# Optimization experiments

Hardware: AMD Instinct MI355X
Metric: run time of the kernel (lower is better)

## Reference

```python
import jax, jax.numpy as jnp
import numpy as np

D_MODEL = 1024
N_HEADS = 16
D_K = D_MODEL // N_HEADS  # 64


def setup_inputs() -> dict:
    key = jax.random.key(0)
    ks = jax.random.split(key, 12)
    B, S = 2, 2048
    inp = {
        "query": jax.random.normal(ks[0], (B, S, D_MODEL), jnp.float32),
        "key": jax.random.normal(ks[1], (B, S, D_MODEL), jnp.float32),
        "value": jax.random.normal(ks[2], (B, S, D_MODEL), jnp.float32),
        "mask": jnp.ones((B, 1, S, S), jnp.int32),
    }
    sc = 1.0 / np.sqrt(D_MODEL)
    inp["Wq"] = jax.random.normal(ks[3], (D_MODEL, D_MODEL), jnp.float32) * sc
    inp["bq"] = jnp.zeros((D_MODEL,), jnp.float32)
    inp["Wk"] = jax.random.normal(ks[4], (D_MODEL, D_MODEL), jnp.float32) * sc
    inp["bk"] = jnp.zeros((D_MODEL,), jnp.float32)
    inp["Wv"] = jax.random.normal(ks[5], (D_MODEL, D_MODEL), jnp.float32) * sc
    inp["bv"] = jnp.zeros((D_MODEL,), jnp.float32)
    inp["Wo"] = jax.random.normal(ks[6], (D_MODEL, D_MODEL), jnp.float32) * sc
    inp["bo"] = jnp.zeros((D_MODEL,), jnp.float32)
    return inp


def reference(query, key, value, mask, Wq, bq, Wk, bk, Wv, bv, Wo, bo):
    B, Sq, _ = query.shape
    H, dk = N_HEADS, D_K
    # linear projections, split heads: (B,S,D) -> (B,H,S,dk)
    def split_heads(x):
        return x.reshape(B, -1, H, dk).transpose(0, 2, 1, 3)
    Q = split_heads(query @ Wq.T + bq)
    K = split_heads(key @ Wk.T + bk)
    V = split_heads(value @ Wv.T + bv)
    scale = 1.0 / jnp.sqrt(jnp.asarray(dk, jnp.float32))
    scores = jnp.einsum('bhqd,bhkd->bhqk', Q, K) * scale
    scores = jnp.where(mask == 0, jnp.asarray(-1e9, scores.dtype), scores)
    attn = jax.nn.softmax(scores, axis=-1)  # (B,H,Sq,Sk)
    out = jnp.einsum('bhqk,bhkd->bhqd', attn, V)
    out = out.transpose(0, 2, 1, 3).reshape(B, Sq, D_MODEL)
    out = out @ Wo.T + bo
    return out, attn
```

## Files before the change

### kernel.cpp

```cpp
#include <hip/hip_runtime.h>
#include <cstdint>
#include <cstddef>

#define DEV __device__ __forceinline__

typedef float f32x4 __attribute__((ext_vector_type(4)));
typedef __bf16 bf16x8 __attribute__((ext_vector_type(8)));
typedef unsigned short u16x8 __attribute__((ext_vector_type(8)));

static constexpr int D = 1024, H = 16, DK = 64, S = 2048, B = 2;
static constexpr int M_TOT = B * S;
static constexpr size_t OUT0 = (size_t)M_TOT * D;

DEV unsigned short f2bf(float f) {
  unsigned x = __builtin_bit_cast(unsigned, f);
  unsigned r = (x + 0x7fffu + ((x >> 16) & 1u)) >> 16;
  return (unsigned short)r;
}

DEV float bf2f(unsigned short u) {
  return __builtin_bit_cast(float, (unsigned)u << 16);
}

DEV f32x4 mfma_bf16(bf16x8 a, bf16x8 b, f32x4 c) {
  return __builtin_amdgcn_mfma_f32_16x16x32_bf16(a, b, c, 0, 0, 0);
}

DEV bf16x8 bc(u16x8 u) { return __builtin_bit_cast(bf16x8, u); }

template <int MODE, bool ABF16>
DEV void proj_body(unsigned short* As, unsigned short* Bs, const void* Aptr,
                   const unsigned short* W, const float* bias, void* dst) {
  constexpr int BM = 128, BK = 32, LDT = 40;
  const int tid = threadIdx.x;
  const int lane = tid & 63, wave = tid >> 6;
  const int wrow = wave >> 1, wcol = wave & 1;
  const int l15 = lane & 15, kg = lane >> 4;
  const int m0 = blockIdx.y * BM, n0 = blockIdx.x * BM;
  const int srow = tid >> 1, scb = (tid & 1) * 16;

  f32x4 acc[4][4] = {};

  for (int kt = 0; kt < D; kt += BK) {
    {
      u16x8 t0, t1;
      if constexpr (ABF16) {
        const unsigned short* ap =
            (const unsigned short*)Aptr + (size_t)(m0 + srow) * D + kt + scb;
        t0 = *(const u16x8*)ap;
        t1 = *(const u16x8*)(ap + 8);
      } else {
        const float* ap = (const float*)Aptr + (size_t)(m0 + srow) * D + kt + scb;
        float4 v0 = *(const float4*)(ap + 0);
        float4 v1 = *(const float4*)(ap + 4);
        float4 v2 = *(const float4*)(ap + 8);
        float4 v3 = *(const float4*)(ap + 12);
        t0[0] = f2bf(v0.x); t0[1] = f2bf(v0.y); t0[2] = f2bf(v0.z); t0[3] = f2bf(v0.w);
        t0[4] = f2bf(v1.x); t0[5] = f2bf(v1.y); t0[6] = f2bf(v1.z); t0[7] = f2bf(v1.w);
        t1[0] = f2bf(v2.x); t1[1] = f2bf(v2.y); t1[2] = f2bf(v2.z); t1[3] = f2bf(v2.w);
        t1[4] = f2bf(v3.x); t1[5] = f2bf(v3.y); t1[6] = f2bf(v3.z); t1[7] = f2bf(v3.w);
      }
      *(u16x8*)&As[srow * LDT + scb] = t0;
      *(u16x8*)&As[srow * LDT + scb + 8] = t1;

      const unsigned short* wp = W + (size_t)(n0 + srow) * D + kt + scb;
      *(u16x8*)&Bs[srow * LDT + scb] = *(const u16x8*)wp;
      *(u16x8*)&Bs[srow * LDT + scb + 8] = *(const u16x8*)(wp + 8);
    }
    __syncthreads();

    bf16x8 a[4], b[4];
#pragma unroll
    for (int i = 0; i < 4; i++)
      a[i] = bc(*(const u16x8*)&As[(wrow * 64 + i * 16 + l15) * LDT + kg * 8]);
#pragma unroll
    for (int i = 0; i < 4; i++)
      b[i] = bc(*(const u16x8*)&Bs[(wcol * 64 + i * 16 + l15) * LDT + kg * 8]);
#pragma unroll
    for (int mi = 0; mi < 4; mi++)
#pragma unroll
      for (int ni = 0; ni < 4; ni++) acc[mi][ni] = mfma_bf16(a[mi], b[ni], acc[mi][ni]);
    __syncthreads();
  }

#pragma unroll
  for (int mi = 0; mi < 4; mi++) {
#pragma unroll
    for (int ni = 0; ni < 4; ni++) {
      const int n = n0 + wcol * 64 + ni * 16 + l15;
      const float bval = bias[n];
#pragma unroll
      for (int r = 0; r < 4; r++) {
        const int m = m0 + wrow * 64 + mi * 16 + kg * 4 + r;
        float v = acc[mi][ni][r] + bval;
        if constexpr (MODE == 0) v *= 0.125f;
        if constexpr (MODE == 0 || MODE == 1) {
          const int b_ = m >> 11, s = m & (S - 1), h = n >> 6, d_ = n & (DK - 1);
          ((unsigned short*)dst)[(((size_t)(b_ * H + h)) * S + s) * DK + d_] = f2bf(v);
        } else if constexpr (MODE == 2) {
          const int b_ = m >> 11, s = m & (S - 1), h = n >> 6, d_ = n & (DK - 1);
          ((unsigned short*)dst)[(((size_t)(b_ * H + h)) * DK + d_) * S + s] = f2bf(v);
        } else {
          ((float*)dst)[(size_t)m * D + n] = v;
        }
      }
    }
  }
}

__global__ __launch_bounds__(256) void conv_kernel(
    const float* __restrict__ Wq, const float* __restrict__ Wk,
    const float* __restrict__ Wv, const float* __restrict__ Wo,
    unsigned short* __restrict__ Wqb, unsigned short* __restrict__ Wkb,
    unsigned short* __restrict__ Wvb, unsigned short* __restrict__ Wob,
    const int* __restrict__ mask, unsigned long long* __restrict__ bits) {
  const int gid = blockIdx.x, tid = threadIdx.x;
  if (gid < 256) {
    const float* srcs[4] = {Wq, Wk, Wv, Wo};
    unsigned short* dsts[4] = {Wqb, Wkb, Wvb, Wob};
    const float* src = srcs[gid >> 6];
    unsigned short* dst = dsts[gid >> 6];
    const size_t off = (size_t)(gid & 63) * 16384;
#pragma unroll
    for (int it = 0; it < 4; it++) {
      const size_t i0 = off + it * 4096 + (size_t)tid * 16;
      float4 v0 = *(const float4*)(src + i0);
      float4 v1 = *(const float4*)(src + i0 + 4);
      float4 v2 = *(const float4*)(src + i0 + 8);
      float4 v3 = *(const float4*)(src + i0 + 12);
      u16x8 t0, t1;
      t0[0] = f2bf(v0.x); t0[1] = f2bf(v0.y); t0[2] = f2bf(v0.z); t0[3] = f2bf(v0.w);
      t0[4] = f2bf(v1.x); t0[5] = f2bf(v1.y); t0[6] = f2bf(v1.z); t0[7] = f2bf(v1.w);
      t1[0] = f2bf(v2.x); t1[1] = f2bf(v2.y); t1[2] = f2bf(v2.z); t1[3] = f2bf(v2.w);
      t1[4] = f2bf(v3.x); t1[5] = f2bf(v3.y); t1[6] = f2bf(v3.z); t1[7] = f2bf(v3.w);
      *(u16x8*)(dst + i0) = t0;
      *(u16x8*)(dst + i0 + 8) = t1;
    }
  } else {
    const int lane = tid & 63;
    const int base = (gid - 256) * 256;
    for (int w = base + (tid >> 6); w < base + 256; w += 4) {
      int m = __builtin_nontemporal_load(mask + (size_t)w * 64 + lane);
      unsigned long long bal = __ballot(m != 0);
      if (lane == 0) bits[w] = bal;
    }
  }
}

struct GemmArgs {
  const float* A[3];
  const unsigned short* Wb[3];
  const float* bias[3];
  unsigned short* dst[3];
};

__global__ __launch_bounds__(256) void qkv_gemm(GemmArgs ga) {
  __shared__ __align__(16) unsigned short As[128 * 40];
  __shared__ __align__(16) unsigned short Bs[128 * 40];
  const int z = blockIdx.z;
  if (z == 0)
    proj_body<0, false>(As, Bs, ga.A[0], ga.Wb[0], ga.bias[0], ga.dst[0]);
  else if (z == 1)
    proj_body<1, false>(As, Bs, ga.A[1], ga.Wb[1], ga.bias[1], ga.dst[1]);
  else
    proj_body<2, false>(As, Bs, ga.A[2], ga.Wb[2], ga.bias[2], ga.dst[2]);
}

__global__ __launch_bounds__(256) void out_proj(const unsigned short* __restrict__ ctx,
                                                const unsigned short* __restrict__ Wob,
                                                const float* __restrict__ bo,
                                                float* __restrict__ out) {
  __shared__ __align__(16) unsigned short As[128 * 40];
  __shared__ __align__(16) unsigned short Bs[128 * 40];
  proj_body<3, true>(As, Bs, ctx, Wob, bo, out);
}

__global__ __launch_bounds__(512, 4) void attn_kernel(
    const unsigned short* __restrict__ Qb, const unsigned short* __restrict__ Kb,
    const unsigned short* __restrict__ Vt, const unsigned* __restrict__ bits32,
    float* __restrict__ attn_out, unsigned short* __restrict__ ctx) {
  constexpr int QB = 32;
  constexpr int PROW = 264;
  __shared__ __align__(16) unsigned short pbuf[2][QB * PROW];
  __shared__ float rsum[8 * QB];
  __shared__ float rinv_s[QB];
  __shared__ unsigned mflag;

  const int wg = blockIdx.x;
  const int qblk = wg & 63, h = (wg >> 6) & 15, b_ = wg >> 10;
  const int bh = b_ * H + h;
  const int qb0 = qblk * QB;
  const int tid = threadIdx.x, lane = tid & 63, wave = tid >> 6;
  const int l15 = lane & 15, kg = lane >> 4;
  const int rowq = kg * 4;
  constexpr float LOG2E = 1.44269504088896340736f;

  const unsigned* mrow = bits32 + ((size_t)b_ * S + qb0) * 64;

  if (tid == 0) mflag = 1u;
  __syncthreads();
  {
    unsigned ok = 1u;
#pragma unroll
    for (int i = 0; i < 4; i++)
      ok &= (mrow[tid + i * 512] == 0xFFFFFFFFu) ? 1u : 0u;
    if (!ok) atomicAnd(&mflag, 0u);
  }

  const unsigned short* qbase = Qb + ((size_t)bh * S + qb0) * DK;
  bf16x8 aq[2][2];
#pragma unroll
  for (int rg = 0; rg < 2; rg++)
#pragma unroll
    for (int hf = 0; hf < 2; hf++)
      aq[rg][hf] =
          bc(*(const u16x8*)(qbase + (size_t)(rg * 16 + l15) * DK + hf * 32 + kg * 8));
  __syncthreads();
  const bool allones = (mflag != 0u);

  float sum[2][4] = {};
#pragma unroll 2
  for (int i = 0; i < 16; i++) {
    const int t = wave * 16 + i;
    const unsigned short* krow = Kb + ((size_t)bh * S + t * 16 + l15) * DK;
    bf16x8 b0 = bc(*(const u16x8*)(krow + kg * 8));
    bf16x8 b1 = bc(*(const u16x8*)(krow + 32 + kg * 8));
    const unsigned shift = (unsigned)((t & 1) * 16 + l15);
#pragma unroll
    for (int rg = 0; rg < 2; rg++) {
      f32x4 c = {0.f, 0.f, 0.f, 0.f};
      c = mfma_bf16(aq[rg][0], b0, c);
      c = mfma_bf16(aq[rg][1], b1, c);
      if (allones) {
#pragma unroll
        for (int r = 0; r < 4; r++) sum[rg][r] += exp2f(c[r] * LOG2E);
      } else {
#pragma unroll
        for (int r = 0; r < 4; r++) {
          const unsigned w = mrow[(rg * 16 + rowq + r) * 64 + (t >> 1)];
          sum[rg][r] += ((w >> shift) & 1u) ? exp2f(c[r] * LOG2E) : 0.f;
        }
      }
    }
  }

#pragma unroll
  for (int rg = 0; rg < 2; rg++)
#pragma unroll
    for (int r = 0; r < 4; r++) {
      float s = sum[rg][r];
      s += __shfl_xor(s, 1);
      s += __shfl_xor(s, 2);
      s += __shfl_xor(s, 4);
      s += __shfl_xor(s, 8);
      if (l15 == 0) rsum[wave * QB + rg * 16 + rowq + r] = s;
    }
  __syncthreads();
  if (tid < QB) {
    float t2 = 0.f;
#pragma unroll
    for (int w = 0; w < 8; w++) t2 += rsum[w * QB + tid];
    rinv_s[tid] = 1.f / t2;
  }
  __syncthreads();

  float ri[2][4];
#pragma unroll
  for (int rg = 0; rg < 2; rg++)
#pragma unroll
    for (int r = 0; r < 4; r++) ri[rg][r] = rinv_s[rg * 16 + rowq + r];

  const int dg = wave & 3, ksub = wave >> 2;
  const unsigned short* vrow = Vt + ((size_t)bh * DK + dg * 16 + l15) * S + ksub * 128;
  float* abase = attn_out + ((size_t)bh * S + qb0) * S;
  const int wrow2 = lane >> 5;
  const int wcol = (lane & 31) * 8;
  f32x4 o[2] = {};

  auto writeDuty = [&](int sbw) {
    const unsigned short* pb = pbuf[sbw & 1];
#pragma unroll
    for (int rr = 0; rr < 2; rr++) {
      const int row = wave * 4 + rr * 2 + wrow2;
      u16x8 u = *(const u16x8*)&pb[row * PROW + wcol];
      f32x4 lo, hi;
      lo[0] = bf2f(u[0]); lo[1] = bf2f(u[1]); lo[2] = bf2f(u[2]); lo[3] = bf2f(u[3]);
      hi[0] = bf2f(u[4]); hi[1] = bf2f(u[5]); hi[2] = bf2f(u[6]); hi[3] = bf2f(u[7]);
      float* dp = abase + (size_t)row * S + sbw * 256 + wcol;
      __builtin_nontemporal_store(lo, (f32x4*)dp);
      __builtin_nontemporal_store(hi, (f32x4*)(dp + 4));
    }
  };

  for (int sb = 0; sb < 8; sb++) {
    if (sb) writeDuty(sb - 1);

    unsigned short* pb = pbuf[sb & 1];
#pragma unroll
    for (int j = 0; j < 2; j++) {
      const int t = sb * 16 + wave * 2 + j;
      const unsigned short* krow = Kb + ((size_t)bh * S + t * 16 + l15) * DK;
      bf16x8 b0 = bc(*(const u16x8*)(krow + kg * 8));
      bf16x8 b1 = bc(*(const u16x8*)(krow + 32 + kg * 8));
      const unsigned shift = (unsigned)((t & 1) * 16 + l15);
      const int lc = (wave * 2 + j) * 16 + l15;
#pragma unroll
      for (int rg = 0; rg < 2; rg++) {
        f32x4 c = {0.f, 0.f, 0.f, 0.f};
        c = mfma_bf16(aq[rg][0], b0, c);
        c = mfma_bf16(aq[rg][1], b1, c);
        if (allones) {
#pragma unroll
          for (int r = 0; r < 4; r++) {
            const int row = rg * 16 + rowq + r;
            pb[row * PROW + lc] = f2bf(exp2f(c[r] * LOG2E) * ri[rg][r]);
          }
        } else {
#pragma unroll
          for (int r = 0; r < 4; r++) {
            const int row = rg * 16 + rowq + r;
            const unsigned w = mrow[row * 64 + (t >> 1)];
            const float e = ((w >> shift) & 1u) ? exp2f(c[r] * LOG2E) : 0.f;
            pb[row * PROW + lc] = f2bf(e * ri[rg][r]);
          }
        }
      }
    }
    __syncthreads();

    const unsigned short* vv = vrow + sb * 256;
#pragma unroll
    for (int ks = 0; ks < 4; ks++) {
      bf16x8 bv = bc(*(const u16x8*)(vv + ks * 32 + kg * 8));
#pragma unroll
      for (int rg = 0; rg < 2; rg++) {
        bf16x8 af = bc(
            *(const u16x8*)&pb[(rg * 16 + l15) * PROW + ksub * 128 + ks * 32 + kg * 8]);
        o[rg] = mfma_bf16(af, bv, o[rg]);
      }
    }
  }
  writeDuty(7);

  float* opart = (float*)&pbuf[0][0];
  __syncthreads();
  if (ksub == 1) {
#pragma unroll
    for (int rg = 0; rg < 2; rg++)
#pragma unroll
      for (int r = 0; r < 4; r++)
        opart[dg * (QB * 17) + (rg * 16 + rowq + r) * 17 + l15] = o[rg][r];
  }
  __syncthreads();
  if (ksub == 0) {
#pragma unroll
    for (int rg = 0; rg < 2; rg++)
#pragma unroll
      for (int r = 0; r < 4; r++) {
        const int row = rg * 16 + rowq + r;
        const float v = o[rg][r] + opart[dg * (QB * 17) + row * 17 + l15];
        ctx[((size_t)(b_ * S + qb0 + row)) * D + h * DK + dg * 16 + l15] = f2bf(v);
      }
  }
}

extern "C" void kernel_launch(void* const* d_in, const int* in_sizes, int n_in,
                              void* d_out, int out_size, void* d_ws, size_t ws_size,
                              hipStream_t stream) {
  const float* query = (const float*)d_in[0];
  const float* key   = (const float*)d_in[1];
  const float* value = (const float*)d_in[2];
  const int*   mask  = (const int*)d_in[3];
  const float* Wq = (const float*)d_in[4];
  const float* bq = (const float*)d_in[5];
  const float* Wk = (const float*)d_in[6];
  const float* bk = (const float*)d_in[7];
  const float* Wv = (const float*)d_in[8];
  const float* bv = (const float*)d_in[9];
  const float* Wo = (const float*)d_in[10];
  const float* bo = (const float*)d_in[11];

  float* out_p = (float*)d_out;
  float* attn_p = (float*)d_out + OUT0;

  size_t off = 0;
  auto carve = [&](size_t bytes) {
    void* p = (char*)d_ws + off;
    off += (bytes + 255) & ~(size_t)255;
    return p;
  };
  const size_t headed = (size_t)B * H * S * DK * sizeof(unsigned short);
  const size_t wbytes = (size_t)D * D * sizeof(unsigned short);
  unsigned short* Qb = (unsigned short*)carve(headed);
  unsigned short* Kb = (unsigned short*)carve(headed);
  unsigned short* Vt = (unsigned short*)carve(headed);
  unsigned short* ctx = (unsigned short*)carve((size_t)M_TOT * D * sizeof(unsigned short));
  unsigned long long* bits = (unsigned long long*)carve((size_t)B * S * S / 8);
  unsigned short* Wqb = (unsigned short*)carve(wbytes);
  unsigned short* Wkb = (unsigned short*)carve(wbytes);
  unsigned short* Wvb = (unsigned short*)carve(wbytes);
  unsigned short* Wob = (unsigned short*)carve(wbytes);

  conv_kernel<<<768, 256, 0, stream>>>(Wq, Wk, Wv, Wo, Wqb, Wkb, Wvb, Wob, mask, bits);

  GemmArgs ga;
  ga.A[0] = query; ga.A[1] = key; ga.A[2] = value;
  ga.Wb[0] = Wqb; ga.Wb[1] = Wkb; ga.Wb[2] = Wvb;
  ga.bias[0] = bq; ga.bias[1] = bk; ga.bias[2] = bv;
  ga.dst[0] = Qb; ga.dst[1] = Kb; ga.dst[2] = Vt;
  qkv_gemm<<<dim3(8, 32, 3), 256, 0, stream>>>(ga);

  attn_kernel<<<B * H * (S / 32), 512, 0, stream>>>(Qb, Kb, Vt, (const unsigned*)bits,
                                                    attn_p, ctx);

  out_proj<<<dim3(8, 32), 256, 0, stream>>>(ctx, Wob, bo, out_p);
}
```

Baseline: 373.9 us.

## Pre-convert QKV activations to bf16 in conv kernel; use lgkm-only barrier in attention

The fp32→bf16 conversion of the query/key/value inputs moves out of the QKV GEMM's tile-load loop and into the existing conversion kernel, which writes bf16 copies to workspace. Each input element was previously converted 8 times (once per N-tile block), and the GEMM read fp32 A tiles, so this removes redundant conversion and halves A-tile load bytes. The cost is an extra write and reread of three 8 MB bf16 buffers. Separately, one __syncthreads in the attention kernel becomes an inline s_waitcnt lgkmcnt(0) plus s_barrier, so the barrier no longer waits on outstanding global memory operations.

Measured after the change: 378.6 us. No clear change (+1.3%).

```diff
diff --git a/kernel.cpp b/kernel.cpp
--- a/kernel.cpp
+++ b/kernel.cpp
@@ -3,6 +3,8 @@
 #include <cstddef>
 
 #define DEV __device__ __forceinline__
+
+#define LGKM_BARRIER() asm volatile("s_waitcnt lgkmcnt(0)\n\ts_barrier" ::: "memory")
 
 typedef float f32x4 __attribute__((ext_vector_type(4)));
 typedef __bf16 bf16x8 __attribute__((ext_vector_type(8)));
@@ -28,9 +30,10 @@
 
 DEV bf16x8 bc(u16x8 u) { return __builtin_bit_cast(bf16x8, u); }
 
-template <int MODE, bool ABF16>
-DEV void proj_body(unsigned short* As, unsigned short* Bs, const void* Aptr,
-                   const unsigned short* W, const float* bias, void* dst) {
+template <int MODE>
+DEV void proj_body(unsigned short* As, unsigned short* Bs,
+                   const unsigned short* A, const unsigned short* W,
+                   const float* bias, void* dst) {
   constexpr int BM = 128, BK = 32, LDT = 40;
   const int tid = threadIdx.x;
   const int lane = tid & 63, wave = tid >> 6;
@@ -43,25 +46,9 @@
 
   for (int kt = 0; kt < D; kt += BK) {
     {
-      u16x8 t0, t1;
-      if constexpr (ABF16) {
-        const unsigned short* ap =
-            (const unsigned short*)Aptr + (size_t)(m0 + srow) * D + kt + scb;
-        t0 = *(const u16x8*)ap;
-        t1 = *(const u16x8*)(ap + 8);
-      } else {
-        const float* ap = (const float*)Aptr + (size_t)(m0 + srow) * D + kt + scb;
-        float4 v0 = *(const float4*)(ap + 0);
-        float4 v1 = *(const float4*)(ap + 4);
-        float4 v2 = *(const float4*)(ap + 8);
-        float4 v3 = *(const float4*)(ap + 12);
-        t0[0] = f2bf(v0.x); t0[1] = f2bf(v0.y); t0[2] = f2bf(v0.z); t0[3] = f2bf(v0.w);
-        t0[4] = f2bf(v1.x); t0[5] = f2bf(v1.y); t0[6] = f2bf(v1.z); t0[7] = f2bf(v1.w);
-        t1[0] = f2bf(v2.x); t1[1] = f2bf(v2.y); t1[2] = f2bf(v2.z); t1[3] = f2bf(v2.w);
-        t1[4] = f2bf(v3.x); t1[5] = f2bf(v3.y); t1[6] = f2bf(v3.z); t1[7] = f2bf(v3.w);
-      }
-      *(u16x8*)&As[srow * LDT + scb] = t0;
-      *(u16x8*)&As[srow * LDT + scb + 8] = t1;
+      const unsigned short* ap = A + (size_t)(m0 + srow) * D + kt + scb;
+      *(u16x8*)&As[srow * LDT + scb] = *(const u16x8*)ap;
+      *(u16x8*)&As[srow * LDT + scb + 8] = *(const u16x8*)(ap + 8);
 
       const unsigned short* wp = W + (size_t)(n0 + srow) * D + kt + scb;
       *(u16x8*)&Bs[srow * LDT + scb] = *(const u16x8*)wp;
@@ -108,19 +95,22 @@
   }
 }
 
-__global__ __launch_bounds__(256) void conv_kernel(
-    const float* __restrict__ Wq, const float* __restrict__ Wk,
-    const float* __restrict__ Wv, const float* __restrict__ Wo,
-    unsigned short* __restrict__ Wqb, unsigned short* __restrict__ Wkb,
-    unsigned short* __restrict__ Wvb, unsigned short* __restrict__ Wob,
-    const int* __restrict__ mask, unsigned long long* __restrict__ bits) {
+struct ConvArgs {
+  const float* src[7];
+  unsigned short* dst[7];
+  const int* mask;
+  unsigned long long* bits;
+};
+
+__global__ __launch_bounds__(256) void conv_kernel(ConvArgs ca) {
   const int gid = blockIdx.x, tid = threadIdx.x;
-  if (gid < 256) {
-    const float* srcs[4] = {Wq, Wk, Wv, Wo};
-    unsigned short* dsts[4] = {Wqb, Wkb, Wvb, Wob};
-    const float* src = srcs[gid >> 6];
-    unsigned short* dst = dsts[gid >> 6];
-    const size_t off = (size_t)(gid & 63) * 16384;
+  if (gid < 1024) {
+    int seg, local;
+    if (gid < 256) { seg = gid >> 6; local = gid & 63; }
+    else { seg = 4 + ((gid - 256) >> 8); local = (gid - 256) & 255; }
+    const float* src = ca.src[seg];
+    unsigned short* dst = ca.dst[seg];
+    const size_t off = (size_t)local * 16384;
 #pragma unroll
     for (int it = 0; it < 4; it++) {
       const size_t i0 = off + it * 4096 + (size_t)tid * 16;
@@ -138,17 +128,17 @@
     }
   } else {
     const int lane = tid & 63;
-    const int base = (gid - 256) * 256;
+    const int base = (gid - 1024) * 256;
     for (int w = base + (tid >> 6); w < base + 256; w += 4) {
-      int m = __builtin_nontemporal_load(mask + (size_t)w * 64 + lane);
+      int m = __builtin_nontemporal_load(ca.mask + (size_t)w * 64 + lane);
       unsigned long long bal = __ballot(m != 0);
-      if (lane == 0) bits[w] = bal;
+      if (lane == 0) ca.bits[w] = bal;
     }
   }
 }
 
 struct GemmArgs {
-  const float* A[3];
+  const unsigned short* Ab[3];
   const unsigned short* Wb[3];
   const float* bias[3];
   unsigned short* dst[3];
@@ -159,11 +149,11 @@
   __shared__ __align__(16) unsigned short Bs[128 * 40];
   const int z = blockIdx.z;
   if (z == 0)
-    proj_body<0, false>(As, Bs, ga.A[0], ga.Wb[0], ga.bias[0], ga.dst[0]);
+    proj_body<0>(As, Bs, ga.Ab[0], ga.Wb[0], ga.bias[0], ga.dst[0]);
   else if (z == 1)
-    proj_body<1, false>(As, Bs, ga.A[1], ga.Wb[1], ga.bias[1], ga.dst[1]);
+    proj_body<1>(As, Bs, ga.Ab[1], ga.Wb[1], ga.bias[1], ga.dst[1]);
   else
-    proj_body<2, false>(As, Bs, ga.A[2], ga.Wb[2], ga.bias[2], ga.dst[2]);
+    proj_body<2>(As, Bs, ga.Ab[2], ga.Wb[2], ga.bias[2], ga.dst[2]);
 }
 
 __global__ __launch_bounds__(256) void out_proj(const unsigned short* __restrict__ ctx,
@@ -172,7 +162,7 @@
                                                 float* __restrict__ out) {
   __shared__ __align__(16) unsigned short As[128 * 40];
   __shared__ __align__(16) unsigned short Bs[128 * 40];
-  proj_body<3, true>(As, Bs, ctx, Wob, bo, out);
+  proj_body<3>(As, Bs, ctx, Wob, bo, out);
 }
 
 __global__ __launch_bounds__(512, 4) void attn_kernel(
@@ -326,7 +316,7 @@
         }
       }
     }
-    __syncthreads();
+    LGKM_BARRIER();
 
     const unsigned short* vv = vrow + sb * 256;
 #pragma unroll
@@ -391,20 +381,30 @@
   };
   const size_t headed = (size_t)B * H * S * DK * sizeof(unsigned short);
   const size_t wbytes = (size_t)D * D * sizeof(unsigned short);
+  const size_t inbytes = (size_t)M_TOT * D * sizeof(unsigned short);
   unsigned short* Qb = (unsigned short*)carve(headed);
   unsigned short* Kb = (unsigned short*)carve(headed);
   unsigned short* Vt = (unsigned short*)carve(headed);
-  unsigned short* ctx = (unsigned short*)carve((size_t)M_TOT * D * sizeof(unsigned short));
+  unsigned short* ctx = (unsigned short*)carve(inbytes);
   unsigned long long* bits = (unsigned long long*)carve((size_t)B * S * S / 8);
   unsigned short* Wqb = (unsigned short*)carve(wbytes);
   unsigned short* Wkb = (unsigned short*)carve(wbytes);
   unsigned short* Wvb = (unsigned short*)carve(wbytes);
   unsigned short* Wob = (unsigned short*)carve(wbytes);
-
-  conv_kernel<<<768, 256, 0, stream>>>(Wq, Wk, Wv, Wo, Wqb, Wkb, Wvb, Wob, mask, bits);
+  unsigned short* Qin = (unsigned short*)carve(inbytes);
+  unsigned short* Kin = (unsigned short*)carve(inbytes);
+  unsigned short* Vin = (unsigned short*)carve(inbytes);
+
+  ConvArgs ca;
+  ca.src[0] = Wq; ca.src[1] = Wk; ca.src[2] = Wv; ca.src[3] = Wo;
+  ca.src[4] = query; ca.src[5] = key; ca.src[6] = value;
+  ca.dst[0] = Wqb; ca.dst[1] = Wkb; ca.dst[2] = Wvb; ca.dst[3] = Wob;
+  ca.dst[4] = Qin; ca.dst[5] = Kin; ca.dst[6] = Vin;
+  ca.mask = mask; ca.bits = bits;
+  conv_kernel<<<1536, 256, 0, stream>>>(ca);
 
   GemmArgs ga;
-  ga.A[0] = query; ga.A[1] = key; ga.A[2] = value;
+  ga.Ab[0] = Qin; ga.Ab[1] = Kin; ga.Ab[2] = Vin;
   ga.Wb[0] = Wqb; ga.Wb[1] = Wkb; ga.Wb[2] = Wvb;
   ga.bias[0] = bq; ga.bias[1] = bk; ga.bias[2] = bv;
   ga.dst[0] = Qb; ga.dst[1] = Kb; ga.dst[2] = Vt;
```
